# Kernel tuning notes

Measured on AMD Instinct MI355X. Metric: run time of the kernel, lower is better.

The kernel has to match this reference:

```python
import jax, jax.numpy as jnp
import numpy as np

NUM_STEPS = 52
HID = 256
NFEAT = 512  # = 2*HID (bidirectional output feeds back as input)
B = 1024


def _lstm_cell(x, h, c, Wih, Whh, bih, bhh):
    # PyTorch gate order: i, f, g, o
    g = x @ Wih.T + h @ Whh.T + bih + bhh  # [B, 4H]
    i, f, gg, o = jnp.split(g, 4, axis=-1)
    i = jax.nn.sigmoid(i)
    f = jax.nn.sigmoid(f)
    gg = jnp.tanh(gg)
    o = jax.nn.sigmoid(o)
    c2 = f * c + i * gg
    h2 = o * jnp.tanh(c2)
    return h2, c2


def setup_inputs() -> dict:
    key = jax.random.key(0)
    ks = jax.random.split(key, 12)
    s = 0.05
    inp = {
        'code': jax.random.normal(ks[0], (B, 2 * 2 * 2 * HID), dtype=jnp.float32),
        'x': jax.random.normal(ks[1], (B, NUM_STEPS, NFEAT), dtype=jnp.float32),
        # layer 0: input size NFEAT; layer 1: input size 2*HID (= NFEAT)
        'W_ih_l0': jax.random.normal(ks[2], (2, 4 * HID, NFEAT), dtype=jnp.float32) * s,
        'W_hh_l0': jax.random.normal(ks[3], (2, 4 * HID, HID), dtype=jnp.float32) * s,
        'b_ih_l0': jax.random.normal(ks[4], (2, 4 * HID), dtype=jnp.float32) * s,
        'b_hh_l0': jax.random.normal(ks[5], (2, 4 * HID), dtype=jnp.float32) * s,
        'W_ih_l1': jax.random.normal(ks[6], (2, 4 * HID, 2 * HID), dtype=jnp.float32) * s,
        'W_hh_l1': jax.random.normal(ks[7], (2, 4 * HID, HID), dtype=jnp.float32) * s,
        'b_ih_l1': jax.random.normal(ks[8], (2, 4 * HID), dtype=jnp.float32) * s,
        'b_hh_l1': jax.random.normal(ks[9], (2, 4 * HID), dtype=jnp.float32) * s,
    }
    return inp


def reference(code, x, W_ih_l0, W_hh_l0, b_ih_l0, b_hh_l0,
              W_ih_l1, W_hh_l1, b_ih_l1, b_hh_l1):
    b = code.shape[0]
    # code -> (h0, c0), each [D*L, B, H] ordered [l0_fwd, l0_bwd, l1_fwd, l1_bwd]
    _code = code.reshape(b, 2, 4, HID)
    h0 = jnp.transpose(_code[:, 0], (1, 0, 2))  # [4, B, H]
    c0 = jnp.transpose(_code[:, 1], (1, 0, 2))
    out0 = jnp.zeros((b, NFEAT), dtype=code.dtype)

    def step(carry, _):
        out, h, c = carry
        # layer 0, both directions (seq_len==1 so fwd/bwd see the same input)
        h0f, c0f = _lstm_cell(out, h[0], c[0], W_ih_l0[0], W_hh_l0[0], b_ih_l0[0], b_hh_l0[0])
        h0b, c0b = _lstm_cell(out, h[1], c[1], W_ih_l0[1], W_hh_l0[1], b_ih_l0[1], b_hh_l0[1])
        x1 = jnp.concatenate([h0f, h0b], axis=-1)  # [B, 2H]
        # layer 1
        h1f, c1f = _lstm_cell(x1, h[2], c[2], W_ih_l1[0], W_hh_l1[0], b_ih_l1[0], b_hh_l1[0])
        h1b, c1b = _lstm_cell(x1, h[3], c[3], W_ih_l1[1], W_hh_l1[1], b_ih_l1[1], b_hh_l1[1])
        y = jnp.concatenate([h1f, h1b], axis=-1)  # [B, 2H] == n_features
        new_h = jnp.stack([h0f, h0b, h1f, h1b])
        new_c = jnp.stack([c0f, c0b, c1f, c1b])
        # output is detached before being fed back (teacher forcing disabled)
        return (jax.lax.stop_gradient(y), new_h, new_c), y

    _, ys = jax.lax.scan(step, (out0, h0, c0), None, length=NUM_STEPS)
    return jnp.transpose(ys, (1, 0, 2))  # [B, num_steps, n_features]
```

## Files before the change

### kernel.cpp

```cpp
#include <hip/hip_runtime.h>
#include <hip/hip_bf16.h>


#define NSTEPS 52

typedef __attribute__((ext_vector_type(8))) short bf16x8;
typedef __attribute__((ext_vector_type(4))) float f32x4;
typedef __attribute__((ext_vector_type(4))) unsigned int u32x4;

__device__ __forceinline__ unsigned short f2bf(float f) {
  union { float f; unsigned int u; } v; v.f = f;
  unsigned int r = v.u + 0x7fffu + ((v.u >> 16) & 1u);
  return (unsigned short)(r >> 16);
}

__device__ __forceinline__ float sigm(float x) { return 1.f / (1.f + __expf(-x)); }
__device__ __forceinline__ float tanh_f(float x) { return 2.f / (1.f + __expf(-2.f * x)) - 1.f; }

__device__ __forceinline__ void async_ld16(const unsigned short* g, unsigned short* l) {
  __builtin_amdgcn_global_load_lds(
      (const __attribute__((address_space(1))) unsigned int*)g,
      (__attribute__((address_space(3))) unsigned int*)l, 16, 0, 0);
}

__global__ void wpack_kernel(const float* __restrict__ Wih0, const float* __restrict__ Whh0,
                             const float* __restrict__ bih0, const float* __restrict__ bhh0,
                             const float* __restrict__ Wih1, const float* __restrict__ Whh1,
                             const float* __restrict__ bih1, const float* __restrict__ bhh1,
                             unsigned short* __restrict__ wpack, float* __restrict__ bsum) {
  int tid = blockIdx.x * 256 + threadIdx.x;
  int lane = tid & 63;
  int chunk = tid >> 6;
  int kc = chunk % 24;
  int cn = chunk / 24;
  int n16 = cn & 63;
  int c = cn >> 6;
  int n = n16 * 16 + (lane & 15);
  int k0 = kc * 32 + (lane >> 4) * 8;
  const float* Wih = (c < 2) ? Wih0 : Wih1;
  const float* Whh = (c < 2) ? Whh0 : Whh1;
  int d = c & 1;
  unsigned short tmp[8];
#pragma unroll
  for (int j = 0; j < 8; j++) {
    int k = k0 + j;
    float val = (k < 512) ? Wih[(d * 1024 + n) * 512 + k]
                          : Whh[(d * 1024 + n) * 256 + (k - 512)];
    tmp[j] = f2bf(val);
  }
  *(u32x4*)(wpack + (size_t)tid * 8) = *(const u32x4*)tmp;
  if (tid < 4096) {
    int c2 = tid >> 10, n2 = tid & 1023;
    float b = (c2 < 2) ? (bih0[(c2 & 1) * 1024 + n2] + bhh0[(c2 & 1) * 1024 + n2])
                       : (bih1[(c2 & 1) * 1024 + n2] + bhh1[(c2 & 1) * 1024 + n2]);
    bsum[tid] = b;
  }
}

__global__ void init_kernel(const float* __restrict__ code,
                            unsigned short* __restrict__ H1, float* __restrict__ C) {
  int t = blockIdx.x * 256 + threadIdx.x;
  int row = t >> 10, col = t & 1023;
  H1[t] = f2bf(code[row * 2048 + col]);
  C[t] = code[row * 2048 + 1024 + col];
}

template <int KC0>
__device__ __forceinline__ void stage_body(
    const unsigned short* __restrict__ Xb, const unsigned short* __restrict__ Hp,
    unsigned short* __restrict__ Hw, float* __restrict__ C,
    const float* __restrict__ bsum, const unsigned short* __restrict__ wpack,
    float* __restrict__ out, int cell0, int step,
    unsigned short* Blds) {
  const int bx = blockIdx.x;
  const int mb = bx & 7;
  const int hsl = (bx >> 3) & 15;
  const int cell = cell0 + (bx >> 7);
  const int tid = threadIdx.x;
  const int lane = tid & 63;
  const int w = tid >> 6;
  const int q = lane >> 4;
  const int ln = lane & 15;

#pragma unroll
  for (int i = 0; i < 12; i++) {
    int ci = w + i * 8;
    int gate = ci & 3, kc = ci >> 2;
    if (kc >= KC0) {
      const unsigned short* gp =
          wpack + ((size_t)((cell * 64 + gate * 16 + hsl) * 24 + kc)) * 512 + lane * 8;
      async_ld16(gp, Blds + (size_t)ci * 512);
    }
  }

  const int arow = (mb * 128 + w * 16 + ln) * 1024 + q * 8;
  bf16x8 afr[24];
#pragma unroll
  for (int kc = KC0; kc < 24; kc++) {
    const unsigned short* ap = (kc < 16) ? (Xb + arow + kc * 32)
                                         : (Hp + arow + cell * 256 + (kc - 16) * 32);
    afr[kc] = *(const bf16x8*)ap;
  }

  f32x4 acc[4];
#pragma unroll
  for (int g = 0; g < 4; g++) acc[g] = (f32x4){0.f, 0.f, 0.f, 0.f};

  __syncthreads();

#pragma unroll
  for (int kc = KC0; kc < 24; kc++) {
#pragma unroll
    for (int g = 0; g < 4; g++) {
      bf16x8 bf = *(const bf16x8*)(Blds + (size_t)(kc * 4 + g) * 512 + lane * 8);
      acc[g] = __builtin_amdgcn_mfma_f32_16x16x32_bf16(afr[kc], bf, acc[g], 0, 0, 0);
    }
  }

  const int colh = hsl * 16 + ln;
  float brg[4];
#pragma unroll
  for (int g = 0; g < 4; g++) brg[g] = bsum[cell * 1024 + g * 256 + colh];

#pragma unroll
  for (int r = 0; r < 4; r++) {
    int row = mb * 128 + w * 16 + q * 4 + r;
    size_t cidx = (size_t)row * 1024 + cell * 256 + colh;
    float cp = C[cidx];
    float iv = sigm(acc[0][r] + brg[0]);
    float fv = sigm(acc[1][r] + brg[1]);
    float gv = tanh_f(acc[2][r] + brg[2]);
    float ov = sigm(acc[3][r] + brg[3]);
    float c2 = fv * cp + iv * gv;
    C[cidx] = c2;
    float hv = ov * tanh_f(c2);
    Hw[cidx] = f2bf(hv);
    if (cell0 == 2)
      out[(size_t)row * (NSTEPS * 512) + step * 512 + (cell - 2) * 256 + colh] = hv;
  }
}

__global__ __launch_bounds__(512, 2) void stage_kernel(
    const unsigned short* __restrict__ Xb, const unsigned short* __restrict__ Hp,
    unsigned short* __restrict__ Hw, float* __restrict__ C,
    const float* __restrict__ bsum, const unsigned short* __restrict__ wpack,
    float* __restrict__ out, int cell0, int step, int kc0) {
  __shared__ unsigned short Blds[96 * 512];
  if (kc0 == 16)
    stage_body<16>(Xb, Hp, Hw, C, bsum, wpack, out, cell0, step, Blds);
  else
    stage_body<0>(Xb, Hp, Hw, C, bsum, wpack, out, cell0, step, Blds);
}

extern "C" void kernel_launch(void* const* d_in, const int* in_sizes, int n_in,
                              void* d_out, int out_size, void* d_ws, size_t ws_size,
                              hipStream_t stream) {
  const float* code = (const float*)d_in[0];
  const float* Wih0 = (const float*)d_in[2];
  const float* Whh0 = (const float*)d_in[3];
  const float* bih0 = (const float*)d_in[4];
  const float* bhh0 = (const float*)d_in[5];
  const float* Wih1 = (const float*)d_in[6];
  const float* Whh1 = (const float*)d_in[7];
  const float* bih1 = (const float*)d_in[8];
  const float* bhh1 = (const float*)d_in[9];

  unsigned short* wpack = (unsigned short*)d_ws;
  float* bsum = (float*)((char*)d_ws + 6291456);
  float* C    = (float*)((char*)d_ws + 6291456 + 16384);
  unsigned short* H0 = (unsigned short*)((char*)d_ws + 6291456 + 16384 + 4194304);
  unsigned short* H1 = H0 + 1024 * 1024;

  float* out = (float*)d_out;

  wpack_kernel<<<1536, 256, 0, stream>>>(Wih0, Whh0, bih0, bhh0,
                                         Wih1, Whh1, bih1, bhh1, wpack, bsum);
  init_kernel<<<4096, 256, 0, stream>>>(code, H1, C);

  for (int t = 0; t < NSTEPS; t++) {
    unsigned short* Hprev = (t & 1) ? H0 : H1;
    unsigned short* Hcur  = (t & 1) ? H1 : H0;
    stage_kernel<<<256, 512, 0, stream>>>(Hprev + 512, Hprev, Hcur, C, bsum, wpack,
                                          out, 0, t, (t == 0) ? 16 : 0);
    stage_kernel<<<256, 512, 0, stream>>>(Hcur, Hprev, Hcur, C, bsum, wpack,
                                          out, 2, t, 0);
  }
}
```

Baseline: 1.544 ms.

## Fuse all LSTM steps into one persistent kernel with per-batch-slice grid barriers

Replaces the 104 per-step kernel launches with a single persistent kernel of 256 blocks. Each block keeps its layer-0 weights resident in LDS, its layer-1 weights in registers, and its cell state in registers. Blocks synchronise through atomic-counter barriers scoped to each batch slice, which removes launch overhead, repeated weight reloads, and C-state round trips through global memory. The risks are spin-wait cost, the need for all 256 blocks to be co-resident (a deadlock otherwise), and higher register and LDS pressure. Layer 1 now runs in four 32-row sub-passes with an LDS exchange buffer.

```diff
diff --git a/kernel.cpp b/kernel.cpp
--- a/kernel.cpp
+++ b/kernel.cpp
@@ -58,98 +58,181 @@
 }
 
 __global__ void init_kernel(const float* __restrict__ code,
-                            unsigned short* __restrict__ H1, float* __restrict__ C) {
+                            unsigned short* __restrict__ H1, float* __restrict__ C,
+                            unsigned int* __restrict__ ctrs) {
   int t = blockIdx.x * 256 + threadIdx.x;
   int row = t >> 10, col = t & 1023;
   H1[t] = f2bf(code[row * 2048 + col]);
   C[t] = code[row * 2048 + 1024 + col];
-}
-
-template <int KC0>
-__device__ __forceinline__ void stage_body(
-    const unsigned short* __restrict__ Xb, const unsigned short* __restrict__ Hp,
-    unsigned short* __restrict__ Hw, float* __restrict__ C,
-    const float* __restrict__ bsum, const unsigned short* __restrict__ wpack,
-    float* __restrict__ out, int cell0, int step,
-    unsigned short* Blds) {
+  if (blockIdx.x == 0 && threadIdx.x < 256) ctrs[threadIdx.x] = 0;
+}
+
+__device__ __forceinline__ void cl_barrier(unsigned int* c, unsigned int expect) {
+  __syncthreads();
+  if (threadIdx.x == 0) {
+    __threadfence();
+    __hip_atomic_fetch_add(c, 1u, __ATOMIC_RELAXED, __HIP_MEMORY_SCOPE_AGENT);
+    while (__hip_atomic_load(c, __ATOMIC_RELAXED, __HIP_MEMORY_SCOPE_AGENT) < expect)
+      __builtin_amdgcn_s_sleep(1);
+    __threadfence();
+  }
+  __syncthreads();
+}
+
+__global__ __launch_bounds__(512, 2) void lstm_persistent(
+    const unsigned short* __restrict__ wpack, const float* __restrict__ bsum,
+    const float* __restrict__ Cg, unsigned short* __restrict__ H0,
+    unsigned short* __restrict__ H1, float* __restrict__ out,
+    unsigned int* __restrict__ ctrs) {
+  __shared__ unsigned short W0[96 * 512];
+  __shared__ unsigned short A1[32 * 768];
+  __shared__ float EX[32 * 65];
+
   const int bx = blockIdx.x;
   const int mb = bx & 7;
   const int hsl = (bx >> 3) & 15;
-  const int cell = cell0 + (bx >> 7);
+  const int p = bx >> 7;
   const int tid = threadIdx.x;
   const int lane = tid & 63;
   const int w = tid >> 6;
   const int q = lane >> 4;
   const int ln = lane & 15;
+  const int g1 = w & 3;
+  const int mh = w >> 2;
+
+  bf16x8 wb1[24];
+#pragma unroll
+  for (int kc = 0; kc < 24; kc++)
+    wb1[kc] = *(const bf16x8*)(
+        wpack + (size_t)((((2 + p) * 64 + g1 * 16 + hsl) * 24 + kc)) * 512 + lane * 8);
 
 #pragma unroll
   for (int i = 0; i < 12; i++) {
     int ci = w + i * 8;
     int gate = ci & 3, kc = ci >> 2;
-    if (kc >= KC0) {
-      const unsigned short* gp =
-          wpack + ((size_t)((cell * 64 + gate * 16 + hsl) * 24 + kc)) * 512 + lane * 8;
-      async_ld16(gp, Blds + (size_t)ci * 512);
-    }
-  }
-
-  const int arow = (mb * 128 + w * 16 + ln) * 1024 + q * 8;
-  bf16x8 afr[24];
-#pragma unroll
-  for (int kc = KC0; kc < 24; kc++) {
-    const unsigned short* ap = (kc < 16) ? (Xb + arow + kc * 32)
-                                         : (Hp + arow + cell * 256 + (kc - 16) * 32);
-    afr[kc] = *(const bf16x8*)ap;
-  }
-
-  f32x4 acc[4];
-#pragma unroll
-  for (int g = 0; g < 4; g++) acc[g] = (f32x4){0.f, 0.f, 0.f, 0.f};
+    async_ld16(wpack + (size_t)(((p * 64 + gate * 16 + hsl) * 24 + kc)) * 512 + lane * 8,
+               W0 + (size_t)ci * 512);
+  }
+
+  const int colh = hsl * 16 + ln;
+  float brg0[4];
+#pragma unroll
+  for (int g = 0; g < 4; g++) brg0[g] = bsum[p * 1024 + g * 256 + colh];
+
+  const int ehid = tid & 15;
+  const int erow = tid >> 4;
+  const int colh1 = hsl * 16 + ehid;
+  float brg1[4];
+#pragma unroll
+  for (int g = 0; g < 4; g++) brg1[g] = bsum[(2 + p) * 1024 + g * 256 + colh1];
+
+  float c0r[4];
+#pragma unroll
+  for (int r = 0; r < 4; r++)
+    c0r[r] = Cg[(size_t)(mb * 128 + w * 16 + q * 4 + r) * 1024 + p * 256 + colh];
+  float c1r[4];
+#pragma unroll
+  for (int qq = 0; qq < 4; qq++)
+    c1r[qq] = Cg[(size_t)(mb * 128 + qq * 32 + erow) * 1024 + (2 + p) * 256 + colh1];
+
+  unsigned int* ctr = ctrs + mb * 32;
+  unsigned int bar = 0;
 
   __syncthreads();
 
-#pragma unroll
-  for (int kc = KC0; kc < 24; kc++) {
-#pragma unroll
-    for (int g = 0; g < 4; g++) {
-      bf16x8 bf = *(const bf16x8*)(Blds + (size_t)(kc * 4 + g) * 512 + lane * 8);
-      acc[g] = __builtin_amdgcn_mfma_f32_16x16x32_bf16(afr[kc], bf, acc[g], 0, 0, 0);
-    }
-  }
-
-  const int colh = hsl * 16 + ln;
-  float brg[4];
-#pragma unroll
-  for (int g = 0; g < 4; g++) brg[g] = bsum[cell * 1024 + g * 256 + colh];
-
-#pragma unroll
-  for (int r = 0; r < 4; r++) {
-    int row = mb * 128 + w * 16 + q * 4 + r;
-    size_t cidx = (size_t)row * 1024 + cell * 256 + colh;
-    float cp = C[cidx];
-    float iv = sigm(acc[0][r] + brg[0]);
-    float fv = sigm(acc[1][r] + brg[1]);
-    float gv = tanh_f(acc[2][r] + brg[2]);
-    float ov = sigm(acc[3][r] + brg[3]);
-    float c2 = fv * cp + iv * gv;
-    C[cidx] = c2;
-    float hv = ov * tanh_f(c2);
-    Hw[cidx] = f2bf(hv);
-    if (cell0 == 2)
-      out[(size_t)row * (NSTEPS * 512) + step * 512 + (cell - 2) * 256 + colh] = hv;
-  }
-}
-
-__global__ __launch_bounds__(512, 2) void stage_kernel(
-    const unsigned short* __restrict__ Xb, const unsigned short* __restrict__ Hp,
-    unsigned short* __restrict__ Hw, float* __restrict__ C,
-    const float* __restrict__ bsum, const unsigned short* __restrict__ wpack,
-    float* __restrict__ out, int cell0, int step, int kc0) {
-  __shared__ unsigned short Blds[96 * 512];
-  if (kc0 == 16)
-    stage_body<16>(Xb, Hp, Hw, C, bsum, wpack, out, cell0, step, Blds);
-  else
-    stage_body<0>(Xb, Hp, Hw, C, bsum, wpack, out, cell0, step, Blds);
+  for (int t = 0; t < NSTEPS; t++) {
+    const unsigned short* __restrict__ Hprev = (t & 1) ? H0 : H1;
+    unsigned short* __restrict__ Hcur = (t & 1) ? H1 : H0;
+
+    f32x4 acc[4];
+#pragma unroll
+    for (int g = 0; g < 4; g++) acc[g] = (f32x4){0.f, 0.f, 0.f, 0.f};
+
+    const int arow = (mb * 128 + w * 16 + ln) * 1024 + q * 8;
+    auto s0chunk = [&](const unsigned short* base, int kcb) {
+      bf16x8 afr[8];
+#pragma unroll
+      for (int kk = 0; kk < 8; kk++) afr[kk] = *(const bf16x8*)(base + kk * 32);
+#pragma unroll
+      for (int kk = 0; kk < 8; kk++) {
+#pragma unroll
+        for (int g = 0; g < 4; g++) {
+          bf16x8 bf = *(const bf16x8*)(W0 + (size_t)((kcb + kk) * 4 + g) * 512 + lane * 8);
+          acc[g] = __builtin_amdgcn_mfma_f32_16x16x32_bf16(afr[kk], bf, acc[g], 0, 0, 0);
+        }
+      }
+    };
+    if (t > 0) {
+      s0chunk(Hprev + arow + 512, 0);
+      s0chunk(Hprev + arow + 512 + 256, 8);
+    }
+    s0chunk(Hprev + arow + p * 256, 16);
+
+#pragma unroll
+    for (int r = 0; r < 4; r++) {
+      float iv = sigm(acc[0][r] + brg0[0]);
+      float fv = sigm(acc[1][r] + brg0[1]);
+      float gv = tanh_f(acc[2][r] + brg0[2]);
+      float ov = sigm(acc[3][r] + brg0[3]);
+      float c2 = fv * c0r[r] + iv * gv;
+      c0r[r] = c2;
+      float hv = ov * tanh_f(c2);
+      Hcur[(size_t)(mb * 128 + w * 16 + q * 4 + r) * 1024 + p * 256 + colh] = f2bf(hv);
+    }
+
+    bar++;
+    cl_barrier(ctr, 32 * bar);
+
+#pragma unroll
+    for (int qq = 0; qq < 4; qq++) {
+#pragma unroll
+      for (int rd = 0; rd < 6; rd++) {
+        int u = rd * 512 + tid;
+        int lrow = u / 96;
+        int k16 = (u % 96) ^ (lrow & 7);
+        int k0 = k16 * 8;
+        int grow = mb * 128 + qq * 32 + lrow;
+        const unsigned short* src =
+            (k0 < 512) ? (Hcur + (size_t)grow * 1024 + k0)
+                       : (Hprev + (size_t)grow * 1024 + 512 + p * 256 + (k0 - 512));
+        async_ld16(src, A1 + (size_t)u * 8);
+      }
+      __syncthreads();
+
+      f32x4 a1acc = (f32x4){0.f, 0.f, 0.f, 0.f};
+      const int lrow = mh * 16 + ln;
+#pragma unroll
+      for (int kc = 0; kc < 24; kc++) {
+        int k16 = ((kc * 4 + q) ^ (lrow & 7));
+        bf16x8 af = *(const bf16x8*)(A1 + (size_t)(lrow * 96 + k16) * 8);
+        a1acc = __builtin_amdgcn_mfma_f32_16x16x32_bf16(af, wb1[kc], a1acc, 0, 0, 0);
+      }
+
+#pragma unroll
+      for (int r = 0; r < 4; r++)
+        EX[(mh * 16 + q * 4 + r) * 65 + g1 * 16 + ln] = a1acc[r];
+      __syncthreads();
+
+      float gvs[4];
+#pragma unroll
+      for (int g = 0; g < 4; g++) gvs[g] = EX[erow * 65 + g * 16 + ehid] + brg1[g];
+      float iv = sigm(gvs[0]);
+      float fv = sigm(gvs[1]);
+      float gg = tanh_f(gvs[2]);
+      float ov = sigm(gvs[3]);
+      float c2 = fv * c1r[qq] + iv * gg;
+      c1r[qq] = c2;
+      float hv = ov * tanh_f(c2);
+      int grow = mb * 128 + qq * 32 + erow;
+      Hcur[(size_t)grow * 1024 + (2 + p) * 256 + colh1] = f2bf(hv);
+      out[(size_t)grow * (NSTEPS * 512) + t * 512 + p * 256 + colh1] = hv;
+    }
+
+    if (t + 1 < NSTEPS) {
+      bar++;
+      cl_barrier(ctr, 32 * bar);
+    }
+  }
 }
 
 extern "C" void kernel_launch(void* const* d_in, const int* in_sizes, int n_in,
@@ -170,19 +253,12 @@
   float* C    = (float*)((char*)d_ws + 6291456 + 16384);
   unsigned short* H0 = (unsigned short*)((char*)d_ws + 6291456 + 16384 + 4194304);
   unsigned short* H1 = H0 + 1024 * 1024;
+  unsigned int* ctrs = (unsigned int*)((char*)d_ws + 14696448);
 
   float* out = (float*)d_out;
 
   wpack_kernel<<<1536, 256, 0, stream>>>(Wih0, Whh0, bih0, bhh0,
                                          Wih1, Whh1, bih1, bhh1, wpack, bsum);
-  init_kernel<<<4096, 256, 0, stream>>>(code, H1, C);
-
-  for (int t = 0; t < NSTEPS; t++) {
-    unsigned short* Hprev = (t & 1) ? H0 : H1;
-    unsigned short* Hcur  = (t & 1) ? H1 : H0;
-    stage_kernel<<<256, 512, 0, stream>>>(Hprev + 512, Hprev, Hcur, C, bsum, wpack,
-                                          out, 0, t, (t == 0) ? 16 : 0);
-    stage_kernel<<<256, 512, 0, stream>>>(Hcur, Hprev, Hcur, C, bsum, wpack,
-                                          out, 2, t, 0);
-  }
-}
+  init_kernel<<<4096, 256, 0, stream>>>(code, H1, C, ctrs);
+  lstm_persistent<<<256, 512, 0, stream>>>(wpack, bsum, C, H0, H1, out, ctrs);
+}
```

Measured after the change: 2.125 ms. 1.38x slower.

## Pipeline weight loads through triple-buffered LDS groups overlapped with MFMA

Applied to the files above, without the earlier changes.

Replaces the single bulk async load of all 96 weight chunks into LDS followed by one barrier with a 3-slot ring of 16-chunk groups. Each group is consumed by MFMAs as soon as its vmcnt wait completes, while later groups are still in flight. Bias and previous cell-state loads are hoisted before the GEMM so their latency overlaps it. LDS shrinks from 96 KB to 48 KB, which may allow more resident blocks. The cost is extra barriers per group and hand-placed waitcnt and setprio instructions that depend on exact counts of outstanding loads.

```diff
diff --git a/kernel.cpp b/kernel.cpp
--- a/kernel.cpp
+++ b/kernel.cpp
@@ -7,6 +7,8 @@
 typedef __attribute__((ext_vector_type(8))) short bf16x8;
 typedef __attribute__((ext_vector_type(4))) float f32x4;
 typedef __attribute__((ext_vector_type(4))) unsigned int u32x4;
+
+template <int I> struct IC { static constexpr int v = I; };
 
 __device__ __forceinline__ unsigned short f2bf(float f) {
   union { float f; unsigned int u; } v; v.f = f;
@@ -82,16 +84,17 @@
   const int q = lane >> 4;
   const int ln = lane & 15;
 
-#pragma unroll
-  for (int i = 0; i < 12; i++) {
-    int ci = w + i * 8;
-    int gate = ci & 3, kc = ci >> 2;
-    if (kc >= KC0) {
-      const unsigned short* gp =
-          wpack + ((size_t)((cell * 64 + gate * 16 + hsl) * 24 + kc)) * 512 + lane * 8;
-      async_ld16(gp, Blds + (size_t)ci * 512);
-    }
-  }
+  constexpr int G0 = KC0 / 4;
+  constexpr int NG = 6 - G0;
+
+  const int colh = hsl * 16 + ln;
+  float brg[4];
+#pragma unroll
+  for (int g = 0; g < 4; g++) brg[g] = bsum[cell * 1024 + g * 256 + colh];
+  float cp[4];
+#pragma unroll
+  for (int r = 0; r < 4; r++)
+    cp[r] = C[(size_t)(mb * 128 + w * 16 + q * 4 + r) * 1024 + cell * 256 + colh];
 
   const int arow = (mb * 128 + w * 16 + ln) * 1024 + q * 8;
   bf16x8 afr[24];
@@ -102,36 +105,65 @@
     afr[kc] = *(const bf16x8*)ap;
   }
 
+  auto issueG = [&](int g) {
+#pragma unroll
+    for (int j = 0; j < 2; j++) {
+      int ci = w * 2 + j;
+      int kcl = ci >> 2, gate = ci & 3;
+      async_ld16(
+          wpack + ((size_t)((cell * 64 + gate * 16 + hsl) * 24 + g * 4 + kcl)) * 512 + lane * 8,
+          Blds + (size_t)((g % 3) * 16 + ci) * 512);
+    }
+  };
+  issueG(G0);
+  if (NG > 1) issueG(G0 + 1);
+  if (NG > 2) issueG(G0 + 2);
+
   f32x4 acc[4];
 #pragma unroll
   for (int g = 0; g < 4; g++) acc[g] = (f32x4){0.f, 0.f, 0.f, 0.f};
 
-  __syncthreads();
-
-#pragma unroll
-  for (int kc = KC0; kc < 24; kc++) {
-#pragma unroll
-    for (int g = 0; g < 4; g++) {
-      bf16x8 bf = *(const bf16x8*)(Blds + (size_t)(kc * 4 + g) * 512 + lane * 8);
-      acc[g] = __builtin_amdgcn_mfma_f32_16x16x32_bf16(afr[kc], bf, acc[g], 0, 0, 0);
+  auto group = [&](auto GI) {
+    constexpr int gi = GI.v;
+    constexpr int g = G0 + gi;
+    constexpr int rem = NG - 1 - gi;
+    constexpr int N = 2 * (rem < 2 ? rem : 2);
+    asm volatile("s_waitcnt vmcnt(%0)" ::"n"(N) : "memory");
+    __builtin_amdgcn_s_barrier();
+    const unsigned short* buf = Blds + (size_t)(g % 3) * 8192;
+    __builtin_amdgcn_s_setprio(1);
+#pragma unroll
+    for (int kcl = 0; kcl < 4; kcl++) {
+#pragma unroll
+      for (int gt = 0; gt < 4; gt++) {
+        bf16x8 bf = *(const bf16x8*)(buf + (size_t)(kcl * 4 + gt) * 512 + lane * 8);
+        acc[gt] = __builtin_amdgcn_mfma_f32_16x16x32_bf16(afr[g * 4 + kcl], bf, acc[gt], 0, 0, 0);
+      }
     }
-  }
-
-  const int colh = hsl * 16 + ln;
-  float brg[4];
-#pragma unroll
-  for (int g = 0; g < 4; g++) brg[g] = bsum[cell * 1024 + g * 256 + colh];
+    __builtin_amdgcn_s_setprio(0);
+    if constexpr (gi < NG - 3) {
+      asm volatile("s_waitcnt lgkmcnt(0)" ::: "memory");
+      __builtin_amdgcn_sched_barrier(0);
+      __builtin_amdgcn_s_barrier();
+      issueG(g + 3);
+    }
+  };
+  group(IC<0>{});
+  if constexpr (NG > 1) group(IC<1>{});
+  if constexpr (NG > 2) group(IC<2>{});
+  if constexpr (NG > 3) group(IC<3>{});
+  if constexpr (NG > 4) group(IC<4>{});
+  if constexpr (NG > 5) group(IC<5>{});
 
 #pragma unroll
   for (int r = 0; r < 4; r++) {
     int row = mb * 128 + w * 16 + q * 4 + r;
     size_t cidx = (size_t)row * 1024 + cell * 256 + colh;
-    float cp = C[cidx];
     float iv = sigm(acc[0][r] + brg[0]);
     float fv = sigm(acc[1][r] + brg[1]);
     float gv = tanh_f(acc[2][r] + brg[2]);
     float ov = sigm(acc[3][r] + brg[3]);
-    float c2 = fv * cp + iv * gv;
+    float c2 = fv * cp[r] + iv * gv;
     C[cidx] = c2;
     float hv = ov * tanh_f(c2);
     Hw[cidx] = f2bf(hv);
@@ -145,7 +177,7 @@
     unsigned short* __restrict__ Hw, float* __restrict__ C,
     const float* __restrict__ bsum, const unsigned short* __restrict__ wpack,
     float* __restrict__ out, int cell0, int step, int kc0) {
-  __shared__ unsigned short Blds[96 * 512];
+  __shared__ unsigned short Blds[3 * 16 * 512];
   if (kc0 == 16)
     stage_body<16>(Xb, Hp, Hw, C, bsum, wpack, out, cell0, step, Blds);
   else
```

Result: faster. 1.473 ms (-4.6%).
